# Kernel optimization log

Hardware: AMD Instinct MI355X
Metric: run time of the kernel (lower is better)

## Reference

```python
import jax, jax.numpy as jnp
import numpy as np

EPS = 1e-8

def _normalize(a):
    return a / jnp.clip(jnp.linalg.norm(a, axis=-1, keepdims=True), EPS)

def _cosine(a, b):
    # pairwise cosine similarity: [Na, d] x [Nb, d] -> [Na, Nb]
    return _normalize(a) @ _normalize(b).T

def setup_inputs() -> dict:
    key = jax.random.key(0)
    n, k, q, d = 100, 5, 75, 4096
    x = jax.random.normal(key, (n * (k + q), d), dtype=jnp.float32)
    tao = jnp.full((1,), 10.0, dtype=jnp.float32)
    return {"x": x, "tao": tao, "n": n, "k": k, "q": q}

def reference(x, tao, n, k, q):
    d = x.shape[-1]
    x = x.reshape(n, k + q, d)
    support = x[:, :k]                      # [n, k, d]
    query = x[:, k:].reshape(n * q, d)      # [NQ, d]
    NQ = n * q
    proto = support.mean(axis=1)            # [n, d]

    pre_sim = _cosine(query, proto)         # [NQ, n]
    pre_label = jnp.argmax(pre_sim, axis=1) # [NQ]

    # vectorized per-class masked softmax aggregation (replaces Python loop)
    cls_ids = jnp.arange(n)
    mask = pre_label[None, :] == cls_ids[:, None]            # [n, NQ]
    logits_q = jnp.where(mask, pre_sim.T, -jnp.inf)          # [n, NQ]
    proto_n = _normalize(proto)
    self_sim = jnp.sum(proto_n * proto_n, axis=-1)           # [n], cosine(proto, proto)
    logits = jnp.concatenate([logits_q, self_sim[:, None]], axis=1)  # [n, NQ+1]
    w = jax.nn.softmax(logits, axis=1)                       # [n, NQ+1]
    adapted_proto = w[:, :NQ] @ query + w[:, NQ:] * proto    # [n, d]

    sim = _cosine(query, adapted_proto)                      # [NQ, n]
    return tao.reshape(()) * sim
```

## Files before the change

### kernel.cpp

```cpp
#include <hip/hip_runtime.h>
#include <hip/hip_bf16.h>
#include <math.h>

#define NQUERY 7500
#define NCLS   100
#define DIM    4096
#define KQ     75
#define KSUP   5
#define RPC    80
#define MPAD   7552
#define NPAD   112
#define CAPQ   256
#define RCAP   2048
#define EPSF   1e-8f
#define SELEM  845824
#define SLICE_BYTES 3383296u

typedef __attribute__((ext_vector_type(8))) short bf16x8;
typedef __attribute__((ext_vector_type(4))) short s16x4;
typedef __attribute__((ext_vector_type(4))) float f32x4;

__device__ __forceinline__ int xrow_of_query(int j) {
    return (j / KQ) * RPC + KSUP + (j % KQ);
}
__device__ __forceinline__ short bf16t(float x) {
    union { float f; unsigned u; } v; v.f = x;
    return (short)(v.u >> 16);
}
__device__ __forceinline__ void gload_lds16(const short* g, short* l) {
    __builtin_amdgcn_global_load_lds(
        (const __attribute__((address_space(1))) unsigned int*)g,
        (__attribute__((address_space(3))) unsigned int*)l, 16, 0, 0);
}

__device__ __forceinline__ size_t tile_off(int nt, int lm, int i) {
    return (((size_t)(nt * 128 + (i >> 5)) * 4 + ((i >> 3) & 3)) * 16 + lm) * 8 + (i & 7);
}

__device__ __forceinline__ void stageB(const short* __restrict__ Bt, int kstep,
        short* buf, int w, int lane) {
#pragma unroll
    for (int p = 0; p < 2; ++p) {
        const int cid = w * 2 + p;
        if (cid < 7) {
            const short* gsrc = Bt + ((size_t)(cid * 128 + kstep) << 9);
            gload_lds16(gsrc + lane * 8, buf + (cid << 9));
        }
    }
}

__global__ __launch_bounds__(256) void k_proto(const float* __restrict__ x,
        float* __restrict__ proto, short* __restrict__ Phi, float* __restrict__ es,
        double* __restrict__ pninv) {
    const int c = blockIdx.x, t = threadIdx.x;
    const int nt = c >> 4, lm = c & 15;
    if (c >= NCLS) {
        for (int g = t; g < 512; g += 256) {
            const int kstep = g >> 2, kq = g & 3;
            size_t o = (((size_t)(nt * 128 + kstep) * 4 + kq) * 16 + lm) * 8;
            bf16x8 z = {0,0,0,0,0,0,0,0};
            *(bf16x8*)(Phi + o) = z;
        }
        if (t == 0) es[c] = 0.f;
        return;
    }
    __shared__ double red[4];
    __shared__ float s_inv;
    const float* b0 = x + (size_t)(c * RPC) * DIM;
    float v[16];
    double ssq = 0.0;
#pragma unroll
    for (int p = 0; p < 4; ++p) {
        const int i = p * 1024 + t * 4;
        f32x4 s = {0.f, 0.f, 0.f, 0.f};
#pragma unroll
        for (int r = 0; r < KSUP; ++r)
            s += *(const f32x4*)(b0 + (size_t)r * DIM + i);
        s = s / 5.0f;
        *(f32x4*)&v[p*4] = s;
        *(f32x4*)(proto + (size_t)c*DIM + i) = s;
        ssq += (double)s[0]*s[0] + (double)s[1]*s[1]
             + (double)s[2]*s[2] + (double)s[3]*s[3];
    }
    for (int o = 32; o; o >>= 1) ssq += __shfl_down(ssq, o);
    if ((t & 63) == 0) red[t >> 6] = ssq;
    __syncthreads();
    if (t == 0) {
        double dtot = red[0] + red[1] + red[2] + red[3];
        pninv[c] = 1.0 / sqrt(dtot);
        float tot = (float)dtot;
        float inv = 1.f / fmaxf(sqrtf(tot), EPSF);
        s_inv = inv;
        es[c] = expf(tot * inv * inv);
    }
    __syncthreads();
    const float inv = s_inv;
#pragma unroll
    for (int p = 0; p < 4; ++p) {
        const int i = p * 1024 + t * 4;
        s16x4 h;
#pragma unroll
        for (int e = 0; e < 4; ++e) h[e] = bf16t(v[p*4+e] * inv);
        *(s16x4*)(Phi + tile_off(nt, lm, i)) = h;
    }
}

template<int TNKS, bool SSQ>
__global__ __launch_bounds__(256) void k_gemm(const float* __restrict__ x,
        const short* __restrict__ Bt, float* __restrict__ Part, float* __restrict__ nq2) {
    constexpr int KST = 128 / TNKS;
    __shared__ short bbuf[2][7 * 512];
    const int bx = blockIdx.x, kz = blockIdx.y;
    const int w = threadIdx.x >> 6, lane = threadIdx.x & 63;
    const int lm = lane & 15, kq = lane >> 4;
    const int mt = bx * 4 + w;
    const int j = mt * 16 + lm;
    const int jc = j < NQUERY ? j : NQUERY - 1;
    const float* pa = x + (size_t)xrow_of_query(jc) * DIM + kq * 8;
    const int ks0 = kz * KST;

    f32x4 acc[7];
#pragma unroll
    for (int nt = 0; nt < 7; ++nt) acc[nt] = (f32x4){0.f,0.f,0.f,0.f};
    float ssq = 0.f;

    stageB(Bt, ks0, bbuf[0], w, lane);
    f32x4 a0 = *(const f32x4*)(pa + ks0 * 32);
    f32x4 a1 = *(const f32x4*)(pa + ks0 * 32 + 4);
    __syncthreads();

#pragma unroll
    for (int s = 0; s < KST; ++s) {
        const int cur = s & 1;
        f32x4 n0 = a0, n1 = a1;
        if (s + 1 < KST) {
            stageB(Bt, ks0 + s + 1, bbuf[cur ^ 1], w, lane);
            n0 = *(const f32x4*)(pa + (ks0 + s + 1) * 32);
            n1 = *(const f32x4*)(pa + (ks0 + s + 1) * 32 + 4);
        }
        float fv[8] = {a0[0],a0[1],a0[2],a0[3],a1[0],a1[1],a1[2],a1[3]};
        bf16x8 ah;
#pragma unroll
        for (int e = 0; e < 8; ++e) {
            if (SSQ) ssq += fv[e] * fv[e];
            ah[e] = bf16t(fv[e]);
        }
#pragma unroll
        for (int nt = 0; nt < 7; ++nt) {
            const bf16x8 bh = *(const bf16x8*)(&bbuf[cur][(nt << 9) + lane * 8]);
            acc[nt] = __builtin_amdgcn_mfma_f32_16x16x32_bf16(ah, bh, acc[nt], 0, 0, 0);
        }
        __syncthreads();
        a0 = n0; a1 = n1;
    }

    if (SSQ) {
        float s2 = ssq;
        s2 += __shfl_xor(s2, 16);
        s2 += __shfl_xor(s2, 32);
        if (kq == 0 && j < NQUERY) atomicAdd(&nq2[j], s2);
    }
    float* sp = Part + (size_t)kz * SELEM + (size_t)(mt * 16) * NPAD;
#pragma unroll
    for (int nt = 0; nt < 7; ++nt)
#pragma unroll
        for (int r = 0; r < 4; ++r)
            sp[(size_t)(kq * 4 + r) * NPAD + nt * 16 + lm] = acc[nt][r];
}

__global__ __launch_bounds__(256) void k_reduce1(const float* __restrict__ Spart,
        float* __restrict__ Sred, int nks) {
    const int idx = blockIdx.x * 256 + threadIdx.x;
    const size_t e = (size_t)idx * 4;
    f32x4 s = {0.f, 0.f, 0.f, 0.f};
    for (int kz = 0; kz < nks; ++kz)
        s += *(const f32x4*)(Spart + (size_t)kz * SELEM + e);
    *(f32x4*)(Sred + e) = s;
}

__global__ __launch_bounds__(256) void k_argmax(const float* __restrict__ S,
        const float* __restrict__ nq2, float* __restrict__ coef, float* __restrict__ invq,
        int* __restrict__ pos, int* __restrict__ ccnt, int* __restrict__ cls_list,
        int* __restrict__ rcnt, int* __restrict__ rlist) {
    const int j = blockIdx.x * 256 + threadIdx.x;
    if (j >= NQUERY) return;
    const float* row = S + (size_t)j * NPAD;
    float m1 = -1e30f, m2 = -1e30f;
    int i1 = 0, i2 = 0;
    for (int c = 0; c < NCLS; ++c) {
        float v = row[c];
        if (v > m1) { m2 = m1; i2 = i1; m1 = v; i1 = c; }
        else if (v > m2) { m2 = v; i2 = c; }
    }
    const float inv = 1.f / fmaxf(sqrtf(nq2[j]), EPSF);
    invq[j] = inv;
    coef[j] = expf(m1 * inv);
    const int p = atomicAdd(&ccnt[i1], 1);
    if (p < CAPQ) { cls_list[i1 * CAPQ + p] = j; pos[j] = p; }
    else pos[j] = -1;
    if ((m1 - m2) * inv < 5e-4f) {
        int rp = atomicAdd(rcnt, 1);
        if (rp < RCAP) rlist[rp] = j | (i1 << 13) | (i2 << 20);
    }
}

__global__ __launch_bounds__(256) void k_refine(const float* __restrict__ x,
        const float* __restrict__ proto, const double* __restrict__ pninv,
        const float* __restrict__ S, const float* __restrict__ invq,
        float* __restrict__ coef, const int* __restrict__ pos,
        int* __restrict__ ccnt, int* __restrict__ cls_list,
        const int* __restrict__ rcnt, const int* __restrict__ rlist) {
    const int cnt = min(*rcnt, RCAP);
    const int t = threadIdx.x;
    __shared__ double red1[4], red2[4];
    for (int e = blockIdx.x; e < cnt; e += gridDim.x) {
        const int pk = rlist[e];
        const int j = pk & 8191, c1 = (pk >> 13) & 127, c2 = (pk >> 20) & 127;
        const float* xq = x + (size_t)xrow_of_query(j) * DIM;
        const float* p1 = proto + (size_t)c1 * DIM;
        const float* p2 = proto + (size_t)c2 * DIM;
        double d1 = 0.0, d2 = 0.0;
        for (int i = t; i < DIM; i += 256) {
            const double qv = (double)xq[i];
            d1 += (double)p1[i] * qv;
            d2 += (double)p2[i] * qv;
        }
        for (int o = 32; o; o >>= 1) { d1 += __shfl_down(d1, o); d2 += __shfl_down(d2, o); }
        if ((t & 63) == 0) { red1[t >> 6] = d1; red2[t >> 6] = d2; }
        __syncthreads();
        if (t == 0) {
            const double cos1 = (red1[0]+red1[1]+red1[2]+red1[3]) * pninv[c1];
            const double cos2 = (red2[0]+red2[1]+red2[2]+red2[3]) * pninv[c2];
            const int win = (cos2 > cos1 || (cos2 == cos1 && c2 < c1)) ? c2 : c1;
            if (win != c1) {
                coef[j] = expf(S[(size_t)j * NPAD + win] * invq[j]);
                const int pj = pos[j];
                if (pj >= 0) cls_list[c1 * CAPQ + pj] = -1;
                const int np = atomicAdd(&ccnt[c2], 1);
                if (np < CAPQ) cls_list[c2 * CAPQ + np] = j;
            }
        }
        __syncthreads();
    }
}

__global__ __launch_bounds__(128) void k_adapt(const float* __restrict__ x,
        const float* __restrict__ coef, const int* __restrict__ cls_cnt,
        const int* __restrict__ cls_list, float* __restrict__ APpart) {
    const int cx = blockIdx.x, c = blockIdx.y, sl = blockIdx.z;
    const int i0 = cx * 512 + threadIdx.x * 4;
    const int n = min(cls_cnt[c], CAPQ);
    f32x4 acc = {0.f, 0.f, 0.f, 0.f};
    for (int e = sl; e < n; e += 4) {
        const int j = cls_list[c * CAPQ + e];
        if (j >= 0) {
            const float cf = coef[j];
            const f32x4 v = *(const f32x4*)(x + (size_t)xrow_of_query(j) * DIM + i0);
            acc += v * cf;
        }
    }
    *(f32x4*)(APpart + (size_t)sl * NCLS * DIM + (size_t)c * DIM + i0) = acc;
}

__global__ __launch_bounds__(256) void k_apnorm(const float* __restrict__ APpart,
        const float* __restrict__ proto, const float* __restrict__ es,
        short* __restrict__ APhi) {
    const int c = blockIdx.x, t = threadIdx.x;
    const int nt = c >> 4, lm = c & 15;
    if (c >= NCLS) {
        for (int g = t; g < 512; g += 256) {
            const int kstep = g >> 2, kq = g & 3;
            size_t o = (((size_t)(nt * 128 + kstep) * 4 + kq) * 16 + lm) * 8;
            bf16x8 z = {0,0,0,0,0,0,0,0};
            *(bf16x8*)(APhi + o) = z;
        }
        return;
    }
    __shared__ float red[4];
    __shared__ float s_inv;
    const float e0 = es[c];
    float v[16];
    float ssq = 0.f;
#pragma unroll
    for (int p = 0; p < 4; ++p) {
        const int i = p * 1024 + t * 4;
        f32x4 s = {0.f, 0.f, 0.f, 0.f};
#pragma unroll
        for (int sl = 0; sl < 4; ++sl)
            s += *(const f32x4*)(APpart + (size_t)sl * NCLS * DIM + (size_t)c * DIM + i);
        f32x4 pr = *(const f32x4*)(proto + (size_t)c*DIM + i);
        s += pr * e0;
        *(f32x4*)&v[p*4] = s;
        ssq += s[0]*s[0] + s[1]*s[1] + s[2]*s[2] + s[3]*s[3];
    }
    for (int o = 32; o; o >>= 1) ssq += __shfl_down(ssq, o);
    if ((t & 63) == 0) red[t >> 6] = ssq;
    __syncthreads();
    if (t == 0) {
        float tot = red[0] + red[1] + red[2] + red[3];
        s_inv = 1.f / fmaxf(sqrtf(tot), EPSF);
    }
    __syncthreads();
    const float inv = s_inv;
#pragma unroll
    for (int p = 0; p < 4; ++p) {
        const int i = p * 1024 + t * 4;
        s16x4 h;
#pragma unroll
        for (int e = 0; e < 4; ++e) h[e] = bf16t(v[p*4+e] * inv);
        *(s16x4*)(APhi + tile_off(nt, lm, i)) = h;
    }
}

__global__ __launch_bounds__(256) void k_reduce2(const float* __restrict__ Opart,
        const float* __restrict__ invq, const float* __restrict__ tao,
        float* __restrict__ out, int nks) {
    const int idx = blockIdx.x * 256 + threadIdx.x;
    if (idx >= NQUERY * 25) return;
    const int j = idx / 25, c4 = (idx % 25) * 4;
    const size_t e = (size_t)j * NPAD + c4;
    f32x4 s = {0.f, 0.f, 0.f, 0.f};
    for (int kz = 0; kz < nks; ++kz)
        s += *(const f32x4*)(Opart + (size_t)kz * SELEM + e);
    const float sc = tao[0] * invq[j];
    *(f32x4*)(out + (size_t)j * NCLS + c4) = s * sc;
}

#define OFF_RCNT   0u
#define OFF_CCNT   256u
#define OFF_NQ2    1792u
#define ZERO_BYTES 32768u
#define OFF_ES     32768u
#define OFF_INVQ   33280u
#define OFF_POS    63488u
#define OFF_COEF   93696u
#define OFF_RLIST  123904u
#define OFF_CLIST  132096u
#define OFF_PNINV  234496u
#define OFF_PROTO  235520u
#define OFF_PHI    1873920u
#define OFF_APHI   2791424u
#define OFF_SRED   3708928u
#define OFF_APPART 7092224u
#define OFF_PART   13645824u

extern "C" void kernel_launch(void* const* d_in, const int* in_sizes, int n_in,
                              void* d_out, int out_size, void* d_ws, size_t ws_size,
                              hipStream_t stream) {
    const float* x   = (const float*)d_in[0];
    const float* tao = (const float*)d_in[1];
    char* ws = (char*)d_ws;

    int*    rcnt    = (int*)   (ws + OFF_RCNT);
    int*    ccnt    = (int*)   (ws + OFF_CCNT);
    float*  nq2     = (float*) (ws + OFF_NQ2);
    float*  es      = (float*) (ws + OFF_ES);
    float*  invq    = (float*) (ws + OFF_INVQ);
    int*    pos     = (int*)   (ws + OFF_POS);
    float*  coef    = (float*) (ws + OFF_COEF);
    int*    rlist   = (int*)   (ws + OFF_RLIST);
    int*    clist   = (int*)   (ws + OFF_CLIST);
    double* pninv   = (double*)(ws + OFF_PNINV);
    float*  proto   = (float*) (ws + OFF_PROTO);
    short*  Phi     = (short*) (ws + OFF_PHI);
    short*  APhi    = (short*) (ws + OFF_APHI);
    float*  Sred    = (float*) (ws + OFF_SRED);
    float*  APpart  = (float*) (ws + OFF_APPART);
    float*  Part    = (float*) (ws + OFF_PART);

    int nks = 1;
    if (ws_size > (size_t)OFF_PART + SLICE_BYTES) {
        size_t avail = (ws_size - OFF_PART) / SLICE_BYTES;
        nks = avail >= 16 ? 16 : (int)avail;
        while (nks & (nks - 1)) nks &= nks - 1;
    }

    hipMemsetAsync(ws, 0, ZERO_BYTES, stream);

    k_proto <<<NPAD, 256, 0, stream>>>(x, proto, Phi, es, pninv);
    switch (nks) {
        case 16: k_gemm<16,true><<<dim3(118, 16), 256, 0, stream>>>(x, Phi, Part, nq2); break;
        case 8:  k_gemm<8, true><<<dim3(118, 8),  256, 0, stream>>>(x, Phi, Part, nq2); break;
        case 4:  k_gemm<4, true><<<dim3(118, 4),  256, 0, stream>>>(x, Phi, Part, nq2); break;
        case 2:  k_gemm<2, true><<<dim3(118, 2),  256, 0, stream>>>(x, Phi, Part, nq2); break;
        default: k_gemm<1, true><<<dim3(118, 1),  256, 0, stream>>>(x, Phi, Part, nq2); break;
    }
    k_reduce1<<<826, 256, 0, stream>>>(Part, Sred, nks);
    k_argmax <<<30, 256, 0, stream>>>(Sred, nq2, coef, invq, pos, ccnt, clist, rcnt, rlist);
    k_refine <<<512, 256, 0, stream>>>(x, proto, pninv, Sred, invq, coef, pos, ccnt, clist, rcnt, rlist);
    k_adapt  <<<dim3(8, NCLS, 4), 128, 0, stream>>>(x, coef, ccnt, clist, APpart);
    k_apnorm <<<NPAD, 256, 0, stream>>>(APpart, proto, es, APhi);
    switch (nks) {
        case 16: k_gemm<16,false><<<dim3(118, 16), 256, 0, stream>>>(x, APhi, Part, nq2); break;
        case 8:  k_gemm<8, false><<<dim3(118, 8),  256, 0, stream>>>(x, APhi, Part, nq2); break;
        case 4:  k_gemm<4, false><<<dim3(118, 4),  256, 0, stream>>>(x, APhi, Part, nq2); break;
        case 2:  k_gemm<2, false><<<dim3(118, 2),  256, 0, stream>>>(x, APhi, Part, nq2); break;
        default: k_gemm<1, false><<<dim3(118, 1),  256, 0, stream>>>(x, APhi, Part, nq2); break;
    }
    k_reduce2<<<733, 256, 0, stream>>>(Part, invq, tao, (float*)d_out, nks);
}
```

Measured before the change: 321.3 us.

## Batch GEMM B staging into 8-step LDS chunks and cache class lists in LDS

The GEMM kernel drops the per-k-step double-buffered B staging with a barrier every step. Each chunk now issues global-to-LDS loads for 8 k-steps and 8 A-register loads at once, then runs 8 steps of MFMAs between barriers. This cuts barrier count and gives more loads in flight, but costs a larger LDS footprint (about 56KB) and more registers, which may lower occupancy and exposes load latency at each chunk start. Separately, k_adapt stages its class list and coefficients into shared memory once per block instead of re-reading them from global memory on every iteration.

```diff
diff --git a/kernel.cpp b/kernel.cpp
--- a/kernel.cpp
+++ b/kernel.cpp
@@ -37,18 +37,6 @@
     return (((size_t)(nt * 128 + (i >> 5)) * 4 + ((i >> 3) & 3)) * 16 + lm) * 8 + (i & 7);
 }
 
-__device__ __forceinline__ void stageB(const short* __restrict__ Bt, int kstep,
-        short* buf, int w, int lane) {
-#pragma unroll
-    for (int p = 0; p < 2; ++p) {
-        const int cid = w * 2 + p;
-        if (cid < 7) {
-            const short* gsrc = Bt + ((size_t)(cid * 128 + kstep) << 9);
-            gload_lds16(gsrc + lane * 8, buf + (cid << 9));
-        }
-    }
-}
-
 __global__ __launch_bounds__(256) void k_proto(const float* __restrict__ x,
         float* __restrict__ proto, short* __restrict__ Phi, float* __restrict__ es,
         double* __restrict__ pninv) {
@@ -109,7 +97,8 @@
 __global__ __launch_bounds__(256) void k_gemm(const float* __restrict__ x,
         const short* __restrict__ Bt, float* __restrict__ Part, float* __restrict__ nq2) {
     constexpr int KST = 128 / TNKS;
-    __shared__ short bbuf[2][7 * 512];
+    constexpr int NCH = KST / 8;
+    __shared__ short sbuf[7 * 8 * 512];
     const int bx = blockIdx.x, kz = blockIdx.y;
     const int w = threadIdx.x >> 6, lane = threadIdx.x & 63;
     const int lm = lane & 15, kq = lane >> 4;
@@ -124,34 +113,40 @@
     for (int nt = 0; nt < 7; ++nt) acc[nt] = (f32x4){0.f,0.f,0.f,0.f};
     float ssq = 0.f;
 
-    stageB(Bt, ks0, bbuf[0], w, lane);
-    f32x4 a0 = *(const f32x4*)(pa + ks0 * 32);
-    f32x4 a1 = *(const f32x4*)(pa + ks0 * 32 + 4);
-    __syncthreads();
-
-#pragma unroll
-    for (int s = 0; s < KST; ++s) {
-        const int cur = s & 1;
-        f32x4 n0 = a0, n1 = a1;
-        if (s + 1 < KST) {
-            stageB(Bt, ks0 + s + 1, bbuf[cur ^ 1], w, lane);
-            n0 = *(const f32x4*)(pa + (ks0 + s + 1) * 32);
-            n1 = *(const f32x4*)(pa + (ks0 + s + 1) * 32 + 4);
-        }
-        float fv[8] = {a0[0],a0[1],a0[2],a0[3],a1[0],a1[1],a1[2],a1[3]};
-        bf16x8 ah;
-#pragma unroll
-        for (int e = 0; e < 8; ++e) {
-            if (SSQ) ssq += fv[e] * fv[e];
-            ah[e] = bf16t(fv[e]);
-        }
-#pragma unroll
-        for (int nt = 0; nt < 7; ++nt) {
-            const bf16x8 bh = *(const bf16x8*)(&bbuf[cur][(nt << 9) + lane * 8]);
-            acc[nt] = __builtin_amdgcn_mfma_f32_16x16x32_bf16(ah, bh, acc[nt], 0, 0, 0);
+#pragma unroll 1
+    for (int cc = 0; cc < NCH; ++cc) {
+        const int kb = ks0 + cc * 8;
+#pragma unroll
+        for (int p = 0; p < 14; ++p) {
+            const int idx = w * 14 + p;
+            const int cid = idx >> 3, s = idx & 7;
+            const short* gsrc = Bt + ((size_t)(cid * 128 + kb + s) << 9);
+            gload_lds16(gsrc + lane * 8, sbuf + ((size_t)idx << 9));
+        }
+        f32x4 A0[8], A1[8];
+#pragma unroll
+        for (int s = 0; s < 8; ++s) {
+            A0[s] = *(const f32x4*)(pa + (size_t)(kb + s) * 32);
+            A1[s] = *(const f32x4*)(pa + (size_t)(kb + s) * 32 + 4);
         }
         __syncthreads();
-        a0 = n0; a1 = n1;
+#pragma unroll
+        for (int s = 0; s < 8; ++s) {
+            float fv[8] = {A0[s][0],A0[s][1],A0[s][2],A0[s][3],
+                           A1[s][0],A1[s][1],A1[s][2],A1[s][3]};
+            bf16x8 ah;
+#pragma unroll
+            for (int e = 0; e < 8; ++e) {
+                if (SSQ) ssq += fv[e] * fv[e];
+                ah[e] = bf16t(fv[e]);
+            }
+#pragma unroll
+            for (int nt = 0; nt < 7; ++nt) {
+                const bf16x8 bh = *(const bf16x8*)(&sbuf[(((size_t)(nt * 8 + s)) << 9) + lane * 8]);
+                acc[nt] = __builtin_amdgcn_mfma_f32_16x16x32_bf16(ah, bh, acc[nt], 0, 0, 0);
+            }
+        }
+        if (cc + 1 < NCH) __syncthreads();
     }
 
     if (SSQ) {
@@ -247,14 +242,22 @@
 __global__ __launch_bounds__(128) void k_adapt(const float* __restrict__ x,
         const float* __restrict__ coef, const int* __restrict__ cls_cnt,
         const int* __restrict__ cls_list, float* __restrict__ APpart) {
+    __shared__ int   s_j[CAPQ];
+    __shared__ float s_cf[CAPQ];
     const int cx = blockIdx.x, c = blockIdx.y, sl = blockIdx.z;
+    const int n = min(cls_cnt[c], CAPQ);
+    for (int e = threadIdx.x; e < n; e += 128) {
+        const int j = cls_list[c * CAPQ + e];
+        s_j[e] = j;
+        s_cf[e] = (j >= 0) ? coef[j] : 0.f;
+    }
+    __syncthreads();
     const int i0 = cx * 512 + threadIdx.x * 4;
-    const int n = min(cls_cnt[c], CAPQ);
     f32x4 acc = {0.f, 0.f, 0.f, 0.f};
     for (int e = sl; e < n; e += 4) {
-        const int j = cls_list[c * CAPQ + e];
+        const int j = s_j[e];
         if (j >= 0) {
-            const float cf = coef[j];
+            const float cf = s_cf[e];
             const f32x4 v = *(const f32x4*)(x + (size_t)xrow_of_query(j) * DIM + i0);
             acc += v * cf;
         }
```

Measured after the change: 323.2 us. No clear change (+0.6%).
